# Performance work log

Measured on AMD Instinct MI355X. Metric: run time of the kernel, lower is better.

Reference implementation:

```python
import jax, jax.numpy as jnp
import numpy as np

N = 100000      # nodes
E = 1600000     # directed edges (avg degree 16)
F_IN, H, C = 128, 64, 40
P_DROP = 0.4144


def gcn_conv(h, row, col, deg_inv_sqrt, W, b):
    # h: [N, d_in] -> [N, d_out]. Symmetric-normalized aggregation with self-loops
    # already folded into (row, col, deg_inv_sqrt).
    h = h @ W                                   # transform first (d_out small)
    norm = deg_inv_sqrt[row] * deg_inv_sqrt[col]  # [E+N]
    msg = h[row] * norm[:, None]                # gather + scale
    out = jax.ops.segment_sum(msg, col, num_segments=N)  # scatter-add
    return out + b


def setup_inputs() -> dict:
    key = jax.random.key(0)
    k1, k2, k3, k4 = jax.random.split(key, 4)
    x = jax.random.normal(k1, (N, F_IN), dtype=jnp.float32)
    edge_index = jax.random.randint(k2, (2, E), 0, N, dtype=jnp.int32)
    W1 = jax.random.normal(k3, (F_IN, H), dtype=jnp.float32) * (1.0 / np.sqrt(F_IN))
    b1 = jnp.zeros((H,), dtype=jnp.float32)
    W2 = jax.random.normal(k4, (H, C), dtype=jnp.float32) * (1.0 / np.sqrt(H))
    b2 = jnp.zeros((C,), dtype=jnp.float32)
    return {"x": x, "edge_index": edge_index, "W1": W1, "b1": b1, "W2": W2, "b2": b2}


def reference(x, edge_index, W1, b1, W2, b2):
    # add self-loops (GCNConv default)
    self_idx = jnp.arange(N, dtype=edge_index.dtype)
    row = jnp.concatenate([edge_index[0], self_idx])
    col = jnp.concatenate([edge_index[1], self_idx])
    deg = jax.ops.segment_sum(jnp.ones_like(col, dtype=x.dtype), col, num_segments=N)
    deg_inv_sqrt = jax.lax.rsqrt(jnp.maximum(deg, 1.0))  # deg >= 1 with self-loops

    h = gcn_conv(x, row, col, deg_inv_sqrt, W1, b1)
    h = jax.nn.relu(h)
    # dropout p=0.4144 with a fixed key (deterministic reference)
    keep = 1.0 - P_DROP
    mask = jax.random.bernoulli(jax.random.key(42), keep, h.shape)
    h = jnp.where(mask, h / keep, 0.0)
    h = gcn_conv(h, row, col, deg_inv_sqrt, W2, b2)
    return jax.nn.log_softmax(h, axis=1)
```

## Files before the change

### kernel.cpp

```cpp
#include <hip/hip_runtime.h>
#include <cstdint>
#include <cstddef>

#define NNODES 100000
#define NEDGES 1600000
#define FIN    128
#define HID    64
#define NCLS   40
#define BSH    9
#define BNODES (1 << BSH)
#define NBUCK  ((NNODES + BNODES - 1) >> BSH)
#define EPB    8192
#define NBINBLK ((NEDGES + EPB - 1) / EPB)
#define CSR_CAP 12288

typedef __attribute__((ext_vector_type(8))) short bf16x8;
typedef __attribute__((ext_vector_type(16))) float f32x16;

__device__ __forceinline__ uint32_t bf16rne(float f) {
  uint32_t u = __float_as_uint(f);
  return (u + 0x7fffu + ((u >> 16) & 1u)) >> 16;
}
__device__ __forceinline__ float bflo(uint32_t u) { return __uint_as_float(u << 16); }
__device__ __forceinline__ float bfhi(uint32_t u) { return __uint_as_float(u & 0xffff0000u); }

__device__ __forceinline__ uint32_t rotl32(uint32_t x, uint32_t r) {
  return (x << r) | (x >> (32u - r));
}

__device__ __forceinline__ void threefry2x32(uint32_t k0, uint32_t k1,
                                             uint32_t c0, uint32_t c1,
                                             uint32_t& o0, uint32_t& o1) {
  const uint32_t ks2 = k0 ^ k1 ^ 0x1BD11BDAu;
  uint32_t x0 = c0 + k0;
  uint32_t x1 = c1 + k1;
#define TF_R(r) { x0 += x1; x1 = rotl32(x1, r); x1 ^= x0; }
  TF_R(13u) TF_R(15u) TF_R(26u) TF_R(6u)
  x0 += k1;  x1 += ks2 + 1u;
  TF_R(17u) TF_R(29u) TF_R(16u) TF_R(24u)
  x0 += ks2; x1 += k0 + 2u;
  TF_R(13u) TF_R(15u) TF_R(26u) TF_R(6u)
  x0 += k0;  x1 += k1 + 3u;
  TF_R(17u) TF_R(29u) TF_R(16u) TF_R(24u)
  x0 += k1;  x1 += ks2 + 4u;
  TF_R(13u) TF_R(15u) TF_R(26u) TF_R(6u)
  x0 += ks2; x1 += k0 + 5u;
#undef TF_R
  o0 = x0; o1 = x1;
}

__global__ __launch_bounds__(256) void k_initcur(int* __restrict__ gcur) {
  gcur[threadIdx.x] = threadIdx.x * CSR_CAP;
}

__global__ __launch_bounds__(256) void k_bin(const int* __restrict__ row,
                                             const int* __restrict__ col,
                                             int* __restrict__ gcur,
                                             uint32_t* __restrict__ pairs) {
  __shared__ int hcnt[256];
  __shared__ int sc[256];
  __shared__ int lofs[256];
  __shared__ int cur2[256];
  __shared__ int gofs[256];
  __shared__ uint32_t buf[EPB];
  __shared__ unsigned char bid[EPB];
  const int t = threadIdx.x;
  const int e0 = blockIdx.x * EPB;
  const int m = min(EPB, NEDGES - e0);
  hcnt[t] = 0;
  __syncthreads();
  for (int i = t; i < m; i += 256) {
    atomicAdd(&hcnt[col[e0 + i] >> BSH], 1);
  }
  __syncthreads();
  sc[t] = hcnt[t];
  __syncthreads();
  for (int d = 1; d < 256; d <<= 1) {
    int u = (t >= d) ? sc[t - d] : 0;
    __syncthreads();
    sc[t] += u;
    __syncthreads();
  }
  const int ex = sc[t] - hcnt[t];
  lofs[t] = ex;
  cur2[t] = ex;
  if (t < NBUCK) gofs[t] = atomicAdd(&gcur[t], hcnt[t]);
  __syncthreads();
  for (int i = t; i < m; i += 256) {
    const int c = col[e0 + i];
    const int r = row[e0 + i];
    const int b = c >> BSH;
    const int p = atomicAdd(&cur2[b], 1);
    buf[p] = ((uint32_t)r << BSH) | (uint32_t)(c & (BNODES - 1));
    bid[p] = (unsigned char)b;
  }
  __syncthreads();
  for (int i = t; i < m; i += 256) {
    const int b = bid[i];
    pairs[gofs[b] + (i - lofs[b])] = buf[i];
  }
}

__global__ __launch_bounds__(256) void k_bscan(const int* __restrict__ gcur,
                                               int* __restrict__ bbase) {
  __shared__ int sc[256];
  __shared__ int cval[256];
  const int t = threadIdx.x;
  const int c = gcur[t] - t * CSR_CAP;
  cval[t] = c;
  sc[t] = c;
  __syncthreads();
  for (int d = 1; d < 256; d <<= 1) {
    int u = (t >= d) ? sc[t - d] : 0;
    __syncthreads();
    sc[t] += u;
    __syncthreads();
  }
  bbase[t] = sc[t] - cval[t];
}

__global__ __launch_bounds__(256) void k_csr(const uint32_t* __restrict__ pairs,
                                             const int* __restrict__ gcur,
                                             const int* __restrict__ bbase,
                                             int* __restrict__ offs,
                                             float* __restrict__ dis,
                                             int* __restrict__ elist) {
  __shared__ int hist[BNODES];
  __shared__ int ncur[BNODES];
  __shared__ int wsum[4];
  __shared__ int ebuf[CSR_CAP];
  const int b = blockIdx.x, t = threadIdx.x;
  const int nf = b << BSH;
  const int slot0 = b * CSR_CAP;
  const int ne = gcur[b] - slot0;
  const int base = bbase[b];
  hist[2 * t] = 0;
  hist[2 * t + 1] = 0;
  __syncthreads();
  for (int i = t; i < ne; i += 256) {
    atomicAdd(&hist[pairs[slot0 + i] & (BNODES - 1)], 1);
  }
  __syncthreads();
  const int a = hist[2 * t], c = hist[2 * t + 1];
  const int s = a + c;
  const int lane = t & 63, wid = t >> 6;
  int scv = s;
#pragma unroll
  for (int off = 1; off < 64; off <<= 1) {
    int u = __shfl_up(scv, off, 64);
    if (lane >= off) scv += u;
  }
  if (lane == 63) wsum[wid] = scv;
  __syncthreads();
  int wadd = 0;
  for (int w = 0; w < wid; ++w) wadd += wsum[w];
  const int ex = scv - s + wadd;
  const int n0 = nf + 2 * t, n1 = nf + 2 * t + 1;
  if (n0 < NNODES) {
    offs[n0] = base + ex;
    dis[n0] = rsqrtf((float)(a + 1));
  }
  if (n1 < NNODES) {
    offs[n1] = base + ex + a;
    dis[n1] = rsqrtf((float)(c + 1));
  }
  if (b == NBUCK - 1 && t == 0) offs[NNODES] = base + ne;
  ncur[2 * t] = ex;
  ncur[2 * t + 1] = ex + a;
  __syncthreads();
  for (int i = t; i < ne; i += 256) {
    const uint32_t p = pairs[slot0 + i];
    const int n = (int)(p & (BNODES - 1));
    const int sl = atomicAdd(&ncur[n], 1);
    ebuf[sl] = (int)(p >> BSH);
  }
  __syncthreads();
  for (int i = t; i < ne; i += 256) elist[base + i] = ebuf[i];
}

__global__ __launch_bounds__(256) void k_mm1(const float* __restrict__ x,
                                             const float* __restrict__ W1,
                                             const float* __restrict__ dis,
                                             ushort* __restrict__ h1s) {
  __shared__ ushort wl[FIN * HID];
  const int t = threadIdx.x;
  for (int i = t; i < FIN * HID; i += 256) wl[i] = (ushort)bf16rne(W1[i]);
  __syncthreads();

  const int lane = t & 63;
  const int wglob = blockIdx.x * 4 + (t >> 6);
  const int r0 = wglob * 64;
  if (r0 >= NNODES) return;
  const int c0 = lane & 31;
  const int hi8 = (lane >> 5) * 8;

  bf16x8 wb0[8], wb1[8];
#pragma unroll
  for (int ks = 0; ks < 8; ++ks) {
#pragma unroll
    for (int i = 0; i < 8; ++i) {
      const int k = ks * 16 + hi8 + i;
      wb0[ks][i] = (short)wl[k * HID + c0];
      wb1[ks][i] = (short)wl[k * HID + 32 + c0];
    }
  }

  const int ra = min(r0 + c0, NNODES - 1);
  const int rb = min(r0 + 32 + c0, NNODES - 1);
  f32x16 acc00 = {0}, acc01 = {0}, acc10 = {0}, acc11 = {0};
#pragma unroll
  for (int ks = 0; ks < 8; ++ks) {
    const int k0 = ks * 16 + hi8;
    const float4 fa0 = *reinterpret_cast<const float4*>(x + (size_t)ra * FIN + k0);
    const float4 fa1 = *reinterpret_cast<const float4*>(x + (size_t)ra * FIN + k0 + 4);
    const float4 fb0 = *reinterpret_cast<const float4*>(x + (size_t)rb * FIN + k0);
    const float4 fb1 = *reinterpret_cast<const float4*>(x + (size_t)rb * FIN + k0 + 4);
    bf16x8 a0, a1;
    a0[0] = (short)bf16rne(fa0.x); a0[1] = (short)bf16rne(fa0.y);
    a0[2] = (short)bf16rne(fa0.z); a0[3] = (short)bf16rne(fa0.w);
    a0[4] = (short)bf16rne(fa1.x); a0[5] = (short)bf16rne(fa1.y);
    a0[6] = (short)bf16rne(fa1.z); a0[7] = (short)bf16rne(fa1.w);
    a1[0] = (short)bf16rne(fb0.x); a1[1] = (short)bf16rne(fb0.y);
    a1[2] = (short)bf16rne(fb0.z); a1[3] = (short)bf16rne(fb0.w);
    a1[4] = (short)bf16rne(fb1.x); a1[5] = (short)bf16rne(fb1.y);
    a1[6] = (short)bf16rne(fb1.z); a1[7] = (short)bf16rne(fb1.w);
    acc00 = __builtin_amdgcn_mfma_f32_32x32x16_bf16(a0, wb0[ks], acc00, 0, 0, 0);
    acc01 = __builtin_amdgcn_mfma_f32_32x32x16_bf16(a0, wb1[ks], acc01, 0, 0, 0);
    acc10 = __builtin_amdgcn_mfma_f32_32x32x16_bf16(a1, wb0[ks], acc10, 0, 0, 0);
    acc11 = __builtin_amdgcn_mfma_f32_32x32x16_bf16(a1, wb1[ks], acc11, 0, 0, 0);
  }

  const int rrb = 4 * (lane >> 5);
#pragma unroll
  for (int reg = 0; reg < 16; ++reg) {
    const int rr = (reg & 3) + 8 * (reg >> 2) + rrb;
    const int r_a = r0 + rr;
    const int r_b = r0 + 32 + rr;
    if (r_a < NNODES) {
      const float d = dis[r_a];
      h1s[(size_t)r_a * HID + c0]      = (ushort)bf16rne(acc00[reg] * d);
      h1s[(size_t)r_a * HID + 32 + c0] = (ushort)bf16rne(acc01[reg] * d);
    }
    if (r_b < NNODES) {
      const float d = dis[r_b];
      h1s[(size_t)r_b * HID + c0]      = (ushort)bf16rne(acc10[reg] * d);
      h1s[(size_t)r_b * HID + 32 + c0] = (ushort)bf16rne(acc11[reg] * d);
    }
  }
}

__global__ __launch_bounds__(256) void k_mm2(const ushort* __restrict__ h2,
                                             const float* __restrict__ W2,
                                             const float* __restrict__ dis,
                                             ushort* __restrict__ gs) {
  __shared__ ushort wl[HID * 64];
  const int t = threadIdx.x;
  for (int i = t; i < HID * 64; i += 256) {
    const int k = i >> 6, c = i & 63;
    wl[i] = (c < NCLS) ? (ushort)bf16rne(W2[k * NCLS + c]) : (ushort)0;
  }
  __syncthreads();

  const int lane = t & 63;
  const int wglob = blockIdx.x * 4 + (t >> 6);
  const int r0 = wglob * 64;
  if (r0 >= NNODES) return;
  const int c0 = lane & 31;
  const int hi8 = (lane >> 5) * 8;

  bf16x8 wb0[4], wb1[4];
#pragma unroll
  for (int ks = 0; ks < 4; ++ks) {
#pragma unroll
    for (int i = 0; i < 8; ++i) {
      const int k = ks * 16 + hi8 + i;
      wb0[ks][i] = (short)wl[k * 64 + c0];
      wb1[ks][i] = (short)wl[k * 64 + 32 + c0];
    }
  }

  const int ra = min(r0 + c0, NNODES - 1);
  const int rb = min(r0 + 32 + c0, NNODES - 1);
  f32x16 acc00 = {0}, acc01 = {0}, acc10 = {0}, acc11 = {0};
#pragma unroll
  for (int ks = 0; ks < 4; ++ks) {
    const int k0 = ks * 16 + hi8;
    const bf16x8 a0 = *reinterpret_cast<const bf16x8*>(h2 + (size_t)ra * HID + k0);
    const bf16x8 a1 = *reinterpret_cast<const bf16x8*>(h2 + (size_t)rb * HID + k0);
    acc00 = __builtin_amdgcn_mfma_f32_32x32x16_bf16(a0, wb0[ks], acc00, 0, 0, 0);
    acc01 = __builtin_amdgcn_mfma_f32_32x32x16_bf16(a0, wb1[ks], acc01, 0, 0, 0);
    acc10 = __builtin_amdgcn_mfma_f32_32x32x16_bf16(a1, wb0[ks], acc10, 0, 0, 0);
    acc11 = __builtin_amdgcn_mfma_f32_32x32x16_bf16(a1, wb1[ks], acc11, 0, 0, 0);
  }

  const int rrb = 4 * (lane >> 5);
#pragma unroll
  for (int reg = 0; reg < 16; ++reg) {
    const int rr = (reg & 3) + 8 * (reg >> 2) + rrb;
    const int r_a = r0 + rr;
    const int r_b = r0 + 32 + rr;
    if (r_a < NNODES) {
      const float d = dis[r_a];
      gs[(size_t)r_a * 64 + c0]      = (ushort)bf16rne(acc00[reg] * d);
      gs[(size_t)r_a * 64 + 32 + c0] = (ushort)bf16rne(acc01[reg] * d);
    }
    if (r_b < NNODES) {
      const float d = dis[r_b];
      gs[(size_t)r_b * 64 + c0]      = (ushort)bf16rne(acc10[reg] * d);
      gs[(size_t)r_b * 64 + 32 + c0] = (ushort)bf16rne(acc11[reg] * d);
    }
  }
}

__global__ __launch_bounds__(256) void k_agg1(const uint32_t* __restrict__ h1u,
                                              const int* __restrict__ elist,
                                              const int* __restrict__ offs,
                                              const float* __restrict__ dis,
                                              const float* __restrict__ b1,
                                              ushort* __restrict__ h2s) {
  const int gid = blockIdx.x * 256 + threadIdx.x;
  const int node = gid >> 6;
  const int lane = gid & 63;
  const int q = lane >> 3, fl = lane & 7;
  const int base = offs[node];
  const int n = offs[node + 1] - base;
  float a0 = 0.f, a1 = 0.f, a2 = 0.f, a3 = 0.f, a4 = 0.f, a5 = 0.f, a6 = 0.f, a7 = 0.f;
  if (q == 0) {
    const uint4 u = *reinterpret_cast<const uint4*>(h1u + (size_t)node * 32 + fl * 4);
    a0 = bflo(u.x); a1 = bfhi(u.x); a2 = bflo(u.y); a3 = bfhi(u.y);
    a4 = bflo(u.z); a5 = bfhi(u.z); a6 = bflo(u.w); a7 = bfhi(u.w);
  }
  for (int k0 = 0; k0 < n; k0 += 64) {
    const int m = min(64, n - k0);
    int srcl = 0;
    if (lane < m) srcl = elist[base + k0 + lane];
    for (int j = 0; j < m; j += 8) {
      const int e = j + q;
      const int s = __shfl(srcl, e, 64);
      if (e < m) {
        const uint4 u = *reinterpret_cast<const uint4*>(h1u + (size_t)s * 32 + fl * 4);
        a0 += bflo(u.x); a1 += bfhi(u.x); a2 += bflo(u.y); a3 += bfhi(u.y);
        a4 += bflo(u.z); a5 += bfhi(u.z); a6 += bflo(u.w); a7 += bfhi(u.w);
      }
    }
  }
#pragma unroll
  for (int off = 8; off < 64; off <<= 1) {
    a0 += __shfl_xor(a0, off, 64); a1 += __shfl_xor(a1, off, 64);
    a2 += __shfl_xor(a2, off, 64); a3 += __shfl_xor(a3, off, 64);
    a4 += __shfl_xor(a4, off, 64); a5 += __shfl_xor(a5, off, 64);
    a6 += __shfl_xor(a6, off, 64); a7 += __shfl_xor(a7, off, 64);
  }
  const int sl = lane >> 3;
  const float v0 = __shfl(a0, sl, 64), v1 = __shfl(a1, sl, 64);
  const float v2 = __shfl(a2, sl, 64), v3 = __shfl(a3, sl, 64);
  const float v4 = __shfl(a4, sl, 64), v5 = __shfl(a5, sl, 64);
  const float v6 = __shfl(a6, sl, 64), v7 = __shfl(a7, sl, 64);
  const int ss = lane & 7;
  float val = (ss == 0) ? v0 : (ss == 1) ? v1 : (ss == 2) ? v2 : (ss == 3) ? v3
            : (ss == 4) ? v4 : (ss == 5) ? v5 : (ss == 6) ? v6 : v7;
  float v = fmaxf(val * dis[node] + b1[lane], 0.0f);
  uint32_t o0, o1;
  threefry2x32(0u, 42u, 0u, (uint32_t)node * HID + lane, o0, o1);
  const uint32_t bits = o0 ^ o1;
  const float u = __uint_as_float((bits >> 9) | 0x3f800000u) - 1.0f;
  const float keepf = (float)(1.0 - 0.4144);
  const float r = (u < keepf) ? v / keepf : 0.0f;
  h2s[(size_t)node * HID + lane] = (ushort)bf16rne(r);
}

__global__ __launch_bounds__(256) void k_agg2(const uint32_t* __restrict__ gsu,
                                              const int* __restrict__ elist,
                                              const int* __restrict__ offs,
                                              const float* __restrict__ dis,
                                              const float* __restrict__ b2,
                                              float* __restrict__ out) {
  const int gid = blockIdx.x * 256 + threadIdx.x;
  const int node = gid >> 6;
  const int lane = gid & 63;
  const int q = lane >> 3, fl = lane & 7;
  const int base = offs[node];
  const int n = offs[node + 1] - base;
  float a0 = 0.f, a1 = 0.f, a2 = 0.f, a3 = 0.f, a4 = 0.f, a5 = 0.f, a6 = 0.f, a7 = 0.f;
  if (q == 0) {
    const uint4 u = *reinterpret_cast<const uint4*>(gsu + (size_t)node * 32 + fl * 4);
    a0 = bflo(u.x); a1 = bfhi(u.x); a2 = bflo(u.y); a3 = bfhi(u.y);
    a4 = bflo(u.z); a5 = bfhi(u.z); a6 = bflo(u.w); a7 = bfhi(u.w);
  }
  for (int k0 = 0; k0 < n; k0 += 64) {
    const int m = min(64, n - k0);
    int srcl = 0;
    if (lane < m) srcl = elist[base + k0 + lane];
    for (int j = 0; j < m; j += 8) {
      const int e = j + q;
      const int s = __shfl(srcl, e, 64);
      if (e < m) {
        const uint4 u = *reinterpret_cast<const uint4*>(gsu + (size_t)s * 32 + fl * 4);
        a0 += bflo(u.x); a1 += bfhi(u.x); a2 += bflo(u.y); a3 += bfhi(u.y);
        a4 += bflo(u.z); a5 += bfhi(u.z); a6 += bflo(u.w); a7 += bfhi(u.w);
      }
    }
  }
#pragma unroll
  for (int off = 8; off < 64; off <<= 1) {
    a0 += __shfl_xor(a0, off, 64); a1 += __shfl_xor(a1, off, 64);
    a2 += __shfl_xor(a2, off, 64); a3 += __shfl_xor(a3, off, 64);
    a4 += __shfl_xor(a4, off, 64); a5 += __shfl_xor(a5, off, 64);
    a6 += __shfl_xor(a6, off, 64); a7 += __shfl_xor(a7, off, 64);
  }
  const int sl = lane >> 3;
  const float v0 = __shfl(a0, sl, 64), v1 = __shfl(a1, sl, 64);
  const float v2 = __shfl(a2, sl, 64), v3 = __shfl(a3, sl, 64);
  const float v4 = __shfl(a4, sl, 64), v5 = __shfl(a5, sl, 64);
  const float v6 = __shfl(a6, sl, 64), v7 = __shfl(a7, sl, 64);
  const int ss = lane & 7;
  float val = (ss == 0) ? v0 : (ss == 1) ? v1 : (ss == 2) ? v2 : (ss == 3) ? v3
            : (ss == 4) ? v4 : (ss == 5) ? v5 : (ss == 6) ? v6 : v7;
  const bool act = lane < NCLS;
  const float l = act ? (val * dis[node] + b2[lane]) : -INFINITY;
  float mx = l;
#pragma unroll
  for (int off = 32; off > 0; off >>= 1) mx = fmaxf(mx, __shfl_xor(mx, off, 64));
  float e = act ? expf(l - mx) : 0.0f;
  float s = e;
#pragma unroll
  for (int off = 32; off > 0; off >>= 1) s += __shfl_xor(s, off, 64);
  const float ls = logf(s);
  if (act) out[(size_t)node * NCLS + lane] = l - mx - ls;
}

extern "C" void kernel_launch(void* const* d_in, const int* in_sizes, int n_in,
                              void* d_out, int out_size, void* d_ws, size_t ws_size,
                              hipStream_t stream) {
  const float* x  = (const float*)d_in[0];
  const int*   ei = (const int*)d_in[1];
  const float* W1 = (const float*)d_in[2];
  const float* b1 = (const float*)d_in[3];
  const float* W2 = (const float*)d_in[4];
  const float* b2 = (const float*)d_in[5];
  float* out = (float*)d_out;

  const int* row = ei;
  const int* col = ei + NEDGES;

  float* ws  = (float*)d_ws;
  float* dis = ws;
  ushort* h1s = (ushort*)(ws + 100352);
  ushort* h2  = h1s + (size_t)NNODES * HID;
  int* offs  = (int*)(h2 + (size_t)NNODES * HID);
  int* gcur  = offs + NNODES + 64;
  int* bbase = gcur + 256;
  int* elist = bbase + 256;
  uint32_t* pairs = (uint32_t*)h1s;
  ushort* gs = h1s;

  const dim3 B(256);
  const int GNW = (NNODES * 64) / 256;
  const int GMM = (NNODES + 255) / 256;

  k_initcur<<<dim3(1), B, 0, stream>>>(gcur);
  k_bin  <<<dim3(NBINBLK), B, 0, stream>>>(row, col, gcur, pairs);
  k_bscan<<<dim3(1), B, 0, stream>>>(gcur, bbase);
  k_csr  <<<dim3(NBUCK), B, 0, stream>>>(pairs, gcur, bbase, offs, dis, elist);

  k_mm1 <<<dim3(GMM), B, 0, stream>>>(x, W1, dis, h1s);
  k_agg1<<<dim3(GNW), B, 0, stream>>>((const uint32_t*)h1s, elist, offs, dis, b1, h2);

  k_mm2 <<<dim3(GMM), B, 0, stream>>>(h2, W2, dis, gs);
  k_agg2<<<dim3(GNW), B, 0, stream>>>((const uint32_t*)gs, elist, offs, dis, b2, out);
}
```

Baseline: 197.6 us.

## Shrink layer-2 row stride to 40, privatize histograms, use wave-scan and nontemporal accesses

Layer-2 transformed features are stored with a 40-column stride instead of 64, so the edge gather in the second aggregation reads 80 bytes per neighbour rather than 128. The binning and CSR histograms are split into per-wave copies to reduce LDS atomic contention. The barrier-heavy block scans are replaced with wavefront shuffle scans. Streaming loads and stores are marked nontemporal. The cost is a few extra LDS adds plus unaligned 16-byte rows and partial lane idleness in the gather.

Result: slower. 213.0 us (+7.8%).

```diff
diff --git a/kernel.cpp b/kernel.cpp
--- a/kernel.cpp
+++ b/kernel.cpp
@@ -57,38 +57,44 @@
                                              const int* __restrict__ col,
                                              int* __restrict__ gcur,
                                              uint32_t* __restrict__ pairs) {
-  __shared__ int hcnt[256];
-  __shared__ int sc[256];
+  __shared__ int hcnt4[4 * 256];
   __shared__ int lofs[256];
   __shared__ int cur2[256];
   __shared__ int gofs[256];
+  __shared__ int wsum[4];
   __shared__ uint32_t buf[EPB];
   __shared__ unsigned char bid[EPB];
   const int t = threadIdx.x;
+  const int lane = t & 63, wid = t >> 6;
   const int e0 = blockIdx.x * EPB;
   const int m = min(EPB, NEDGES - e0);
-  hcnt[t] = 0;
+#pragma unroll
+  for (int i = 0; i < 4; ++i) hcnt4[i * 256 + t] = 0;
   __syncthreads();
   for (int i = t; i < m; i += 256) {
-    atomicAdd(&hcnt[col[e0 + i] >> BSH], 1);
-  }
-  __syncthreads();
-  sc[t] = hcnt[t];
-  __syncthreads();
-  for (int d = 1; d < 256; d <<= 1) {
-    int u = (t >= d) ? sc[t - d] : 0;
-    __syncthreads();
-    sc[t] += u;
-    __syncthreads();
-  }
-  const int ex = sc[t] - hcnt[t];
+    const int c = __builtin_nontemporal_load(col + e0 + i);
+    atomicAdd(&hcnt4[wid * 256 + (c >> BSH)], 1);
+  }
+  __syncthreads();
+  const int h = hcnt4[t] + hcnt4[256 + t] + hcnt4[512 + t] + hcnt4[768 + t];
+  int sc = h;
+#pragma unroll
+  for (int off = 1; off < 64; off <<= 1) {
+    int u = __shfl_up(sc, off, 64);
+    if (lane >= off) sc += u;
+  }
+  if (lane == 63) wsum[wid] = sc;
+  __syncthreads();
+  int wadd = 0;
+  for (int w = 0; w < wid; ++w) wadd += wsum[w];
+  const int ex = sc - h + wadd;
   lofs[t] = ex;
   cur2[t] = ex;
-  if (t < NBUCK) gofs[t] = atomicAdd(&gcur[t], hcnt[t]);
+  if (t < NBUCK) gofs[t] = atomicAdd(&gcur[t], h);
   __syncthreads();
   for (int i = t; i < m; i += 256) {
-    const int c = col[e0 + i];
-    const int r = row[e0 + i];
+    const int c = __builtin_nontemporal_load(col + e0 + i);
+    const int r = __builtin_nontemporal_load(row + e0 + i);
     const int b = c >> BSH;
     const int p = atomicAdd(&cur2[b], 1);
     buf[p] = ((uint32_t)r << BSH) | (uint32_t)(c & (BNODES - 1));
@@ -103,20 +109,20 @@
 
 __global__ __launch_bounds__(256) void k_bscan(const int* __restrict__ gcur,
                                                int* __restrict__ bbase) {
-  __shared__ int sc[256];
-  __shared__ int cval[256];
-  const int t = threadIdx.x;
+  __shared__ int wsum[4];
+  const int t = threadIdx.x, lane = t & 63, wid = t >> 6;
   const int c = gcur[t] - t * CSR_CAP;
-  cval[t] = c;
-  sc[t] = c;
-  __syncthreads();
-  for (int d = 1; d < 256; d <<= 1) {
-    int u = (t >= d) ? sc[t - d] : 0;
-    __syncthreads();
-    sc[t] += u;
-    __syncthreads();
-  }
-  bbase[t] = sc[t] - cval[t];
+  int sc = c;
+#pragma unroll
+  for (int off = 1; off < 64; off <<= 1) {
+    int u = __shfl_up(sc, off, 64);
+    if (lane >= off) sc += u;
+  }
+  if (lane == 63) wsum[wid] = sc;
+  __syncthreads();
+  int wadd = 0;
+  for (int w = 0; w < wid; ++w) wadd += wsum[w];
+  bbase[t] = sc - c + wadd;
 }
 
 __global__ __launch_bounds__(256) void k_csr(const uint32_t* __restrict__ pairs,
@@ -125,7 +131,7 @@
                                              int* __restrict__ offs,
                                              float* __restrict__ dis,
                                              int* __restrict__ elist) {
-  __shared__ int hist[BNODES];
+  __shared__ int hist4[4 * BNODES];
   __shared__ int ncur[BNODES];
   __shared__ int wsum[4];
   __shared__ int ebuf[CSR_CAP];
@@ -134,16 +140,16 @@
   const int slot0 = b * CSR_CAP;
   const int ne = gcur[b] - slot0;
   const int base = bbase[b];
-  hist[2 * t] = 0;
-  hist[2 * t + 1] = 0;
+  const int lane = t & 63, wid = t >> 6;
+  for (int i = t; i < 4 * BNODES; i += 256) hist4[i] = 0;
   __syncthreads();
   for (int i = t; i < ne; i += 256) {
-    atomicAdd(&hist[pairs[slot0 + i] & (BNODES - 1)], 1);
-  }
-  __syncthreads();
-  const int a = hist[2 * t], c = hist[2 * t + 1];
+    atomicAdd(&hist4[wid * BNODES + (pairs[slot0 + i] & (BNODES - 1))], 1);
+  }
+  __syncthreads();
+  const int a = hist4[2 * t] + hist4[BNODES + 2 * t] + hist4[2 * BNODES + 2 * t] + hist4[3 * BNODES + 2 * t];
+  const int c = hist4[2 * t + 1] + hist4[BNODES + 2 * t + 1] + hist4[2 * BNODES + 2 * t + 1] + hist4[3 * BNODES + 2 * t + 1];
   const int s = a + c;
-  const int lane = t & 63, wid = t >> 6;
   int scv = s;
 #pragma unroll
   for (int off = 1; off < 64; off <<= 1) {
@@ -294,6 +300,7 @@
   }
 
   const int rrb = 4 * (lane >> 5);
+  const bool c1ok = c0 < (NCLS - 32);
 #pragma unroll
   for (int reg = 0; reg < 16; ++reg) {
     const int rr = (reg & 3) + 8 * (reg >> 2) + rrb;
@@ -301,13 +308,13 @@
     const int r_b = r0 + 32 + rr;
     if (r_a < NNODES) {
       const float d = dis[r_a];
-      gs[(size_t)r_a * 64 + c0]      = (ushort)bf16rne(acc00[reg] * d);
-      gs[(size_t)r_a * 64 + 32 + c0] = (ushort)bf16rne(acc01[reg] * d);
+      gs[(size_t)r_a * NCLS + c0] = (ushort)bf16rne(acc00[reg] * d);
+      if (c1ok) gs[(size_t)r_a * NCLS + 32 + c0] = (ushort)bf16rne(acc01[reg] * d);
     }
     if (r_b < NNODES) {
       const float d = dis[r_b];
-      gs[(size_t)r_b * 64 + c0]      = (ushort)bf16rne(acc10[reg] * d);
-      gs[(size_t)r_b * 64 + 32 + c0] = (ushort)bf16rne(acc11[reg] * d);
+      gs[(size_t)r_b * NCLS + c0] = (ushort)bf16rne(acc10[reg] * d);
+      if (c1ok) gs[(size_t)r_b * NCLS + 32 + c0] = (ushort)bf16rne(acc11[reg] * d);
     }
   }
 }
@@ -333,7 +340,7 @@
   for (int k0 = 0; k0 < n; k0 += 64) {
     const int m = min(64, n - k0);
     int srcl = 0;
-    if (lane < m) srcl = elist[base + k0 + lane];
+    if (lane < m) srcl = __builtin_nontemporal_load(elist + base + k0 + lane);
     for (int j = 0; j < m; j += 8) {
       const int e = j + q;
       const int s = __shfl(srcl, e, 64);
@@ -366,7 +373,7 @@
   const float u = __uint_as_float((bits >> 9) | 0x3f800000u) - 1.0f;
   const float keepf = (float)(1.0 - 0.4144);
   const float r = (u < keepf) ? v / keepf : 0.0f;
-  h2s[(size_t)node * HID + lane] = (ushort)bf16rne(r);
+  __builtin_nontemporal_store((ushort)bf16rne(r), h2s + (size_t)node * HID + lane);
 }
 
 __global__ __launch_bounds__(256) void k_agg2(const uint32_t* __restrict__ gsu,
@@ -379,23 +386,24 @@
   const int node = gid >> 6;
   const int lane = gid & 63;
   const int q = lane >> 3, fl = lane & 7;
+  const bool ldq = fl < 5;
   const int base = offs[node];
   const int n = offs[node + 1] - base;
   float a0 = 0.f, a1 = 0.f, a2 = 0.f, a3 = 0.f, a4 = 0.f, a5 = 0.f, a6 = 0.f, a7 = 0.f;
-  if (q == 0) {
-    const uint4 u = *reinterpret_cast<const uint4*>(gsu + (size_t)node * 32 + fl * 4);
+  if (q == 0 && ldq) {
+    const uint4 u = *reinterpret_cast<const uint4*>(gsu + (size_t)node * 20 + fl * 4);
     a0 = bflo(u.x); a1 = bfhi(u.x); a2 = bflo(u.y); a3 = bfhi(u.y);
     a4 = bflo(u.z); a5 = bfhi(u.z); a6 = bflo(u.w); a7 = bfhi(u.w);
   }
   for (int k0 = 0; k0 < n; k0 += 64) {
     const int m = min(64, n - k0);
     int srcl = 0;
-    if (lane < m) srcl = elist[base + k0 + lane];
+    if (lane < m) srcl = __builtin_nontemporal_load(elist + base + k0 + lane);
     for (int j = 0; j < m; j += 8) {
       const int e = j + q;
       const int s = __shfl(srcl, e, 64);
-      if (e < m) {
-        const uint4 u = *reinterpret_cast<const uint4*>(gsu + (size_t)s * 32 + fl * 4);
+      if (ldq && e < m) {
+        const uint4 u = *reinterpret_cast<const uint4*>(gsu + (size_t)s * 20 + fl * 4);
         a0 += bflo(u.x); a1 += bfhi(u.x); a2 += bflo(u.y); a3 += bfhi(u.y);
         a4 += bflo(u.z); a5 += bfhi(u.z); a6 += bflo(u.w); a7 += bfhi(u.w);
       }
@@ -426,7 +434,7 @@
 #pragma unroll
   for (int off = 32; off > 0; off >>= 1) s += __shfl_xor(s, off, 64);
   const float ls = logf(s);
-  if (act) out[(size_t)node * NCLS + lane] = l - mx - ls;
+  if (act) __builtin_nontemporal_store(l - mx - ls, out + (size_t)node * NCLS + lane);
 }
 
 extern "C" void kernel_launch(void* const* d_in, const int* in_sizes, int n_in,
```
